# Kernel tuning notes

Measured on AMD Instinct MI355X. Metric: run time of the kernel, lower is better.

Reference implementation:

```python
import jax, jax.numpy as jnp
import numpy as np


def _highway(x, Ws, bs):
    # Ws: [n_hw, 2H, H] (torch Linear layout), bs: [n_hw, 2H]
    H = x.shape[-1]
    for i in range(Ws.shape[0]):
        proj = jnp.einsum('bsh,oh->bso', x, Ws[i]) + bs[i]
        nonlin = jax.nn.relu(proj[..., :H])
        gate = jax.nn.sigmoid(proj[..., H:])
        x = gate * x + (1.0 - gate) * nonlin
    return x


def setup_inputs() -> dict:
    key = jax.random.key(0)
    ks = jax.random.split(key, 10)
    B, S, H, L, W, NHW = 32, 512, 512, 2, 4, 2
    scale = 1.0 / np.sqrt(H)
    return {
        'inputs': jax.random.normal(ks[0], (B, S, H), dtype=jnp.float32),
        'masks': jnp.ones((B, S), dtype=jnp.int32),
        'fwd_pads': jax.random.normal(ks[1], (L, W, H), dtype=jnp.float32) * scale,
        'bwd_pads': jax.random.normal(ks[2], (L, W, H), dtype=jnp.float32) * scale,
        'fwd_ws': jax.random.normal(ks[3], (L, W + 1), dtype=jnp.float32),
        'bwd_ws': jax.random.normal(ks[4], (L, W + 1), dtype=jnp.float32),
        'fwd_hw_W': jax.random.normal(ks[5], (L, NHW, 2 * H, H), dtype=jnp.float32) * scale,
        'fwd_hw_b': jax.random.normal(ks[6], (L, NHW, 2 * H), dtype=jnp.float32) * 0.1,
        'bwd_hw_W': jax.random.normal(ks[7], (L, NHW, 2 * H, H), dtype=jnp.float32) * scale,
        'bwd_hw_b': jax.random.normal(ks[8], (L, NHW, 2 * H), dtype=jnp.float32) * 0.1,
    }


def reference(inputs, masks, fwd_pads, bwd_pads, fwd_ws, bwd_ws,
              fwd_hw_W, fwd_hw_b, bwd_hw_W, bwd_hw_b):
    # inputs: [B,S,H]; masks unused (as in the torch module)
    B, S, H = inputs.shape
    L, W, _ = fwd_pads.shape
    fwd_in = inputs
    bwd_in = inputs
    outs = []
    for l in range(L):
        fp = jnp.broadcast_to(fwd_pads[l], (B, W, H))
        bp = jnp.broadcast_to(bwd_pads[l], (B, W, H))
        pf = jnp.concatenate([fp, fwd_in, bp], axis=1)  # [B, S+2W, H]
        pb = jnp.concatenate([fp, bwd_in, bp], axis=1)
        # forward window at t covers padded positions t..t+W (causal)
        f_win = jnp.stack([pf[:, k:k + S] for k in range(W + 1)], axis=0)  # [W+1,B,S,H]
        f_out = jnp.einsum('k,kbsh->bsh', fwd_ws[l], f_win)
        # backward window at t covers padded positions t+W..t+2W (anti-causal)
        b_win = jnp.stack([pb[:, W + k:W + k + S] for k in range(W + 1)], axis=0)
        b_out = jnp.einsum('k,kbsh->bsh', bwd_ws[l], b_win)
        f_out = _highway(f_out, fwd_hw_W[l], fwd_hw_b[l])
        b_out = _highway(b_out, bwd_hw_W[l], bwd_hw_b[l])
        fwd_in, bwd_in = f_out, b_out
        outs.append(jnp.concatenate([f_out, b_out], axis=-1))
    return jnp.stack(outs, axis=0)  # [L, B, S, 2H]
```

## Files before the change

### kernel.cpp

```cpp
#include <hip/hip_runtime.h>
#include <hip/hip_bf16.h>

typedef __attribute__((ext_vector_type(8))) short bf16x8;
typedef __attribute__((ext_vector_type(4))) float floatx4;

#define B_ 32
#define S_ 512
#define H_ 512
#define M_ (B_*S_)
#define K_ 512
#define N_ 1024

__device__ __forceinline__ void gload_lds16(const void* g, void* l) {
  __builtin_amdgcn_global_load_lds(
      (const __attribute__((address_space(1))) void*)g,
      (__attribute__((address_space(3))) void*)l, 16, 0, 0);
}

__global__ void cvt_kernel(const float* __restrict__ src,
                           __hip_bfloat16* __restrict__ dst, int n4) {
  int t = blockIdx.x * 256 + threadIdx.x;
  if (t >= n4) return;
  float4 v = *(const float4*)(src + (size_t)t * 4);
  union { ushort4 u; __hip_bfloat16 h[4]; } pk;
  pk.h[0] = __float2bfloat16(v.x);
  pk.h[1] = __float2bfloat16(v.y);
  pk.h[2] = __float2bfloat16(v.z);
  pk.h[3] = __float2bfloat16(v.w);
  *(ushort4*)((unsigned short*)dst + (size_t)t * 4) = pk.u;
}

__global__ void conv_kernel(const float* __restrict__ inf, const float* __restrict__ inb,
                            int instride,
                            const float* __restrict__ fpad, const float* __restrict__ bpad,
                            const float* __restrict__ fw, const float* __restrict__ bw,
                            __hip_bfloat16* __restrict__ xaf, __hip_bfloat16* __restrict__ xab) {
  int t = blockIdx.x * 256 + threadIdx.x;
  int dir = blockIdx.y;
  int row = t >> 7;
  int hv  = (t & 127) << 2;
  int s = row & (S_ - 1);
  float4 a = make_float4(0.f, 0.f, 0.f, 0.f);
  if (dir == 0) {
#pragma unroll
    for (int k = 0; k < 5; ++k) {
      float w = fw[k];
      const float* src = (s + k < 4) ? (fpad + (size_t)(s + k) * H_ + hv)
                                     : (inf + (size_t)(row + k - 4) * instride + hv);
      float4 v = *(const float4*)src;
      a.x += w * v.x; a.y += w * v.y; a.z += w * v.z; a.w += w * v.w;
    }
  } else {
#pragma unroll
    for (int k = 0; k < 5; ++k) {
      float w = bw[k];
      const float* src = (s + k < S_) ? (inb + (size_t)(row + k) * instride + hv)
                                      : (bpad + (size_t)(s + k - S_) * H_ + hv);
      float4 v = *(const float4*)src;
      a.x += w * v.x; a.y += w * v.y; a.z += w * v.z; a.w += w * v.w;
    }
  }
  __hip_bfloat16* xa = dir ? xab : xaf;
  union { ushort4 u; __hip_bfloat16 h[4]; } pk;
  pk.h[0] = __float2bfloat16(a.x);
  pk.h[1] = __float2bfloat16(a.y);
  pk.h[2] = __float2bfloat16(a.z);
  pk.h[3] = __float2bfloat16(a.w);
  *(ushort4*)((unsigned short*)xa + (size_t)row * H_ + hv) = pk.u;
}

__global__ void hw_gemm(const __hip_bfloat16* __restrict__ Af, const __hip_bfloat16* __restrict__ Ab,
                        const __hip_bfloat16* __restrict__ Wf, const __hip_bfloat16* __restrict__ Wb,
                        const float* __restrict__ biasf, const float* __restrict__ biasb,
                        __hip_bfloat16* __restrict__ Anf, __hip_bfloat16* __restrict__ Anb,
                        float* __restrict__ outp, int final_mode) {
  __shared__ __align__(16) __hip_bfloat16 lA[128 * 64];
  __shared__ __align__(16) __hip_bfloat16 lB[128 * 64];

  const int tid = threadIdx.x;
  const int lane = tid & 63, wave = tid >> 6;
  const int wm = wave >> 1, wn = wave & 1;
  const int quad = lane >> 4, l16 = lane & 15;
  const int h0 = blockIdx.x * 64;
  const int m0 = blockIdx.y * 128;
  const int dir = blockIdx.z;

  const __hip_bfloat16* A = dir ? Ab : Af;
  const __hip_bfloat16* Wm = dir ? Wb : Wf;
  const float* bias = dir ? biasb : biasf;
  __hip_bfloat16* An = dir ? Anb : Anf;

  floatx4 acc[4][4];
#pragma unroll
  for (int i = 0; i < 4; ++i)
#pragma unroll
    for (int j = 0; j < 4; ++j) acc[i][j] = (floatx4){0.f, 0.f, 0.f, 0.f};

  float xs[4][2][4];

  const int srow = lane >> 3;
  const int skk  = (lane & 7) * 8;
  const int xkp = h0 >> 6;

  for (int kp = 0; kp < 8; ++kp) {
    const int kb = kp * 64;
#pragma unroll
    for (int c = 0; c < 4; ++c) {
      int chunk = wave * 4 + c;
      int arow = chunk * 8 + srow;
      gload_lds16(A + (size_t)(m0 + arow) * K_ + kb + skk, &lA[chunk * 512]);
    }
#pragma unroll
    for (int c = 0; c < 4; ++c) {
      int chunk = wave * 4 + c;
      int brow = chunk * 8 + srow;
      int wrow = (brow < 64) ? (h0 + brow) : (512 + h0 + brow - 64);
      gload_lds16(Wm + (size_t)wrow * K_ + kb + skk, &lB[chunk * 512]);
    }
    __syncthreads();

    if (kp == xkp) {
#pragma unroll
      for (int i = 0; i < 4; ++i)
#pragma unroll
        for (int j = 0; j < 2; ++j)
#pragma unroll
          for (int r = 0; r < 4; ++r)
            xs[i][j][r] = __bfloat162float(
                lA[(wm * 64 + i * 16 + quad * 4 + r) * 64 + wn * 32 + j * 16 + l16]);
    }

#pragma unroll
    for (int ks = 0; ks < 2; ++ks) {
      const int ko = ks * 32 + quad * 8;
      bf16x8 av[4], bv[4];
#pragma unroll
      for (int i = 0; i < 4; ++i)
        av[i] = *(const bf16x8*)&lA[(wm * 64 + i * 16 + l16) * 64 + ko];
#pragma unroll
      for (int j = 0; j < 2; ++j)
        bv[j] = *(const bf16x8*)&lB[(wn * 32 + j * 16 + l16) * 64 + ko];
#pragma unroll
      for (int j = 0; j < 2; ++j)
        bv[2 + j] = *(const bf16x8*)&lB[(64 + wn * 32 + j * 16 + l16) * 64 + ko];
#pragma unroll
      for (int i = 0; i < 4; ++i)
#pragma unroll
        for (int j = 0; j < 4; ++j)
          acc[i][j] = __builtin_amdgcn_mfma_f32_16x16x32_bf16(av[i], bv[j], acc[i][j], 0, 0, 0);
    }
    __syncthreads();
  }

  const int cbase = h0 + wn * 32 + l16;
  float bnl[2], bgt[2];
#pragma unroll
  for (int j = 0; j < 2; ++j) {
    bnl[j] = bias[cbase + j * 16];
    bgt[j] = bias[512 + cbase + j * 16];
  }
#pragma unroll
  for (int i = 0; i < 4; ++i) {
    const int rbase = m0 + wm * 64 + i * 16 + quad * 4;
#pragma unroll
    for (int r = 0; r < 4; ++r) {
      const int row = rbase + r;
#pragma unroll
      for (int j = 0; j < 2; ++j) {
        const int c = cbase + j * 16;
        float pn = acc[i][j][r] + bnl[j];
        float pg = acc[i][j + 2][r] + bgt[j];
        float g = 1.f / (1.f + __expf(-pg));
        float xo = xs[i][j][r];
        float xn = g * xo + (1.f - g) * fmaxf(pn, 0.f);
        if (final_mode) {
          outp[(size_t)row * N_ + dir * H_ + c] = xn;
        } else {
          An[(size_t)row * H_ + c] = __float2bfloat16(xn);
        }
      }
    }
  }
}

extern "C" void kernel_launch(void* const* d_in, const int* in_sizes, int n_in,
                              void* d_out, int out_size, void* d_ws, size_t ws_size,
                              hipStream_t stream) {
  const float* inputs   = (const float*)d_in[0];
  const float* fwd_pads = (const float*)d_in[2];
  const float* bwd_pads = (const float*)d_in[3];
  const float* fwd_ws_p = (const float*)d_in[4];
  const float* bwd_ws_p = (const float*)d_in[5];
  const float* fwd_hw_W = (const float*)d_in[6];
  const float* fwd_hw_b = (const float*)d_in[7];
  const float* bwd_hw_W = (const float*)d_in[8];
  const float* bwd_hw_b = (const float*)d_in[9];
  float* out = (float*)d_out;

  char* ws = (char*)d_ws;
  size_t off = 0;
  __hip_bfloat16* Wbf = (__hip_bfloat16*)(ws + off); off += (size_t)4194304 * 2;
  __hip_bfloat16* xa0f = (__hip_bfloat16*)(ws + off); off += (size_t)M_ * H_ * 2;
  __hip_bfloat16* xa0b = (__hip_bfloat16*)(ws + off); off += (size_t)M_ * H_ * 2;
  __hip_bfloat16* xa1f = (__hip_bfloat16*)(ws + off); off += (size_t)M_ * H_ * 2;
  __hip_bfloat16* xa1b = (__hip_bfloat16*)(ws + off); off += (size_t)M_ * H_ * 2;

  cvt_kernel<<<2048, 256, 0, stream>>>(fwd_hw_W, Wbf, 524288);
  cvt_kernel<<<2048, 256, 0, stream>>>(bwd_hw_W, Wbf + (size_t)2097152, 524288);

  for (int l = 0; l < 2; ++l) {
    const float *inf, *inb;
    int instride;
    if (l == 0) { inf = inputs; inb = inputs; instride = H_; }
    else        { inf = out;    inb = out + H_; instride = N_; }
    conv_kernel<<<dim3(8192, 2), 256, 0, stream>>>(
        inf, inb, instride,
        fwd_pads + (size_t)l * 4 * H_, bwd_pads + (size_t)l * 4 * H_,
        fwd_ws_p + l * 5, bwd_ws_p + l * 5,
        xa0f, xa0b);

    hw_gemm<<<dim3(8, 128, 2), 256, 0, stream>>>(
        xa0f, xa0b,
        Wbf + (size_t)(l * 2) * 524288, Wbf + (size_t)2097152 + (size_t)(l * 2) * 524288,
        fwd_hw_b + (l * 2) * 1024, bwd_hw_b + (l * 2) * 1024,
        xa1f, xa1b, nullptr, 0);

    hw_gemm<<<dim3(8, 128, 2), 256, 0, stream>>>(
        xa1f, xa1b,
        Wbf + (size_t)(l * 2 + 1) * 524288, Wbf + (size_t)2097152 + (size_t)(l * 2 + 1) * 524288,
        fwd_hw_b + (l * 2 + 1) * 1024, bwd_hw_b + (l * 2 + 1) * 1024,
        nullptr, nullptr, out + (size_t)l * M_ * N_, 1);
  }
}
```

Baseline: 479.6 us.

## Swizzle LDS tiles with XOR layout and remap blocks across XCDs

Applies an XOR swizzle to the 16-byte chunk column when async-loading A and W tiles into LDS, and matches it in the MFMA operand reads and the residual x reads, to remove LDS bank conflicts on the row-strided bf16x8 loads. Remaps the block index so that blocks assigned round-robin to the same XCD share M rows (A tiles), which should improve L2 reuse. Also hoists the global load pointers out of the k loop. The swizzle must stay consistent between the writes and every read path.

```diff
diff --git a/kernel.cpp b/kernel.cpp
--- a/kernel.cpp
+++ b/kernel.cpp
@@ -81,9 +81,12 @@
   const int lane = tid & 63, wave = tid >> 6;
   const int wm = wave >> 1, wn = wave & 1;
   const int quad = lane >> 4, l16 = lane & 15;
-  const int h0 = blockIdx.x * 64;
-  const int m0 = blockIdx.y * 128;
   const int dir = blockIdx.z;
+
+  const int n = blockIdx.y * 8 + blockIdx.x;
+  const int xcd = n & 7;
+  const int h0 = ((n >> 3) & 7) * 64;
+  const int m0 = (xcd + (n >> 6) * 8) * 128;
 
   const __hip_bfloat16* A = dir ? Ab : Af;
   const __hip_bfloat16* Wm = dir ? Wb : Wf;
@@ -99,23 +102,29 @@
   float xs[4][2][4];
 
   const int srow = lane >> 3;
-  const int skk  = (lane & 7) * 8;
-  const int xkp = h0 >> 6;
+  const int skk  = (((lane & 7) ^ srow) << 3);
+  const int xkp  = h0 >> 6;
+  const int sw   = l16 & 7;
+
+  const __hip_bfloat16* aptr[4];
+  const __hip_bfloat16* bptr[4];
+#pragma unroll
+  for (int c = 0; c < 4; ++c) {
+    const int chunk = wave * 4 + c;
+    const int arow = chunk * 8 + srow;
+    aptr[c] = A + (size_t)(m0 + arow) * K_ + skk;
+    const int brow = chunk * 8 + srow;
+    const int wrow = (brow < 64) ? (h0 + brow) : (512 + h0 + brow - 64);
+    bptr[c] = Wm + (size_t)wrow * K_ + skk;
+  }
 
   for (int kp = 0; kp < 8; ++kp) {
     const int kb = kp * 64;
 #pragma unroll
     for (int c = 0; c < 4; ++c) {
-      int chunk = wave * 4 + c;
-      int arow = chunk * 8 + srow;
-      gload_lds16(A + (size_t)(m0 + arow) * K_ + kb + skk, &lA[chunk * 512]);
-    }
-#pragma unroll
-    for (int c = 0; c < 4; ++c) {
-      int chunk = wave * 4 + c;
-      int brow = chunk * 8 + srow;
-      int wrow = (brow < 64) ? (h0 + brow) : (512 + h0 + brow - 64);
-      gload_lds16(Wm + (size_t)wrow * K_ + kb + skk, &lB[chunk * 512]);
+      const int chunk = wave * 4 + c;
+      gload_lds16(aptr[c] + kb, &lA[chunk * 512]);
+      gload_lds16(bptr[c] + kb, &lB[chunk * 512]);
     }
     __syncthreads();
 
@@ -125,24 +134,32 @@
 #pragma unroll
         for (int j = 0; j < 2; ++j)
 #pragma unroll
-          for (int r = 0; r < 4; ++r)
+          for (int r = 0; r < 4; ++r) {
+            const int ra = wm * 64 + i * 16 + quad * 4 + r;
+            const int c2 = wn * 32 + j * 16 + l16;
             xs[i][j][r] = __bfloat162float(
-                lA[(wm * 64 + i * 16 + quad * 4 + r) * 64 + wn * 32 + j * 16 + l16]);
+                lA[ra * 64 + ((((c2 >> 3) ^ (ra & 7)) << 3) | (c2 & 7))]);
+          }
     }
 
 #pragma unroll
     for (int ks = 0; ks < 2; ++ks) {
-      const int ko = ks * 32 + quad * 8;
       bf16x8 av[4], bv[4];
 #pragma unroll
-      for (int i = 0; i < 4; ++i)
-        av[i] = *(const bf16x8*)&lA[(wm * 64 + i * 16 + l16) * 64 + ko];
-#pragma unroll
-      for (int j = 0; j < 2; ++j)
-        bv[j] = *(const bf16x8*)&lB[(wn * 32 + j * 16 + l16) * 64 + ko];
-#pragma unroll
-      for (int j = 0; j < 2; ++j)
-        bv[2 + j] = *(const bf16x8*)&lB[(64 + wn * 32 + j * 16 + l16) * 64 + ko];
+      for (int i = 0; i < 4; ++i) {
+        const int ra = wm * 64 + i * 16 + l16;
+        av[i] = *(const bf16x8*)&lA[ra * 64 + (((ks * 4 + quad) ^ sw) << 3)];
+      }
+#pragma unroll
+      for (int j = 0; j < 2; ++j) {
+        const int rb = wn * 32 + j * 16 + l16;
+        bv[j] = *(const bf16x8*)&lB[rb * 64 + (((ks * 4 + quad) ^ sw) << 3)];
+      }
+#pragma unroll
+      for (int j = 0; j < 2; ++j) {
+        const int rb = 64 + wn * 32 + j * 16 + l16;
+        bv[2 + j] = *(const bf16x8*)&lB[rb * 64 + (((ks * 4 + quad) ^ sw) << 3)];
+      }
 #pragma unroll
       for (int i = 0; i < 4; ++i)
 #pragma unroll
```

New measurement: 474.3 us. Within noise of the previous version (-1.1%).
